# Optimization experiments

Hardware: AMD Instinct MI355X
Metric: run time of the kernel (lower is better)

## Reference

```python
import jax, jax.numpy as jnp
import numpy as np

KW = 3          # kernel_width
PAD = (KW - 1) // 2


def setup_inputs() -> dict:
    key = jax.random.key(0)
    ks = jax.random.split(key, 7)
    B, QL, KL, QS, KS = 16, 1024, 1024, 512, 512
    q = jax.random.normal(ks[0], (B, QL, QS), dtype=jnp.float32)
    k = jax.random.normal(ks[1], (B, KL, KS), dtype=jnp.float32)
    # torch Linear weights: [out_features, in_features]
    Wk = jax.random.normal(ks[2], (KS * KW, QS), dtype=jnp.float32) * (1.0 / np.sqrt(QS))
    bk = jax.random.normal(ks[3], (KS * KW,), dtype=jnp.float32) * 0.02
    Wb = jax.random.normal(ks[4], (1, QS), dtype=jnp.float32) * (1.0 / np.sqrt(QS))
    bb = jax.random.normal(ks[5], (1,), dtype=jnp.float32) * 0.02
    bias_b = jax.random.normal(ks[6], (1,), dtype=jnp.float32)
    return {"q": q, "k": k, "Wk": Wk, "bk": bk, "Wb": Wb, "bb": bb, "bias_b": bias_b}


def reference(q, k, Wk, bk, Wb, bb, bias_b):
    B, QL, QS = q.shape
    _, KL, KS = k.shape
    # per-query dynamic kernels: [B, QL, KS, KW]
    kernel = (jnp.einsum('biq,oq->bio', q, Wk) + bk).reshape(B, QL, KS, KW)
    # per-query scalar bias: [B, QL]
    bias = (jnp.einsum('biq,oq->bio', q, Wb) + bb)[..., 0]
    # banded multiply-accumulate, equivalent to grouped conv1d with groups=B
    k_pad = jnp.pad(k, ((0, 0), (PAD, PAD), (0, 0)))  # [B, KL+KW-1, KS]
    # windows[b, j, t, c] = k_pad[b, j+t, c]  -> [B, KL, KW, KS]
    windows = jnp.stack([k_pad[:, t:t + KL, :] for t in range(KW)], axis=2)
    scores = jnp.einsum('bict,bjtc->bij', kernel, windows)
    return scores + bias[:, :, None] + bias_b[0]
```

## Files before the change

kernel.cpp:

```cpp
#include <hip/hip_runtime.h>

typedef unsigned short ushort_t;
typedef unsigned int uint32;
typedef __bf16 bf16x8 __attribute__((ext_vector_type(8)));
typedef float f32x4 __attribute__((ext_vector_type(4)));
typedef float f4 __attribute__((ext_vector_type(4)));
typedef unsigned short us4 __attribute__((ext_vector_type(4)));


__device__ __forceinline__ ushort_t f2bf(float f) {
    uint32 u = __builtin_bit_cast(uint32, f);
    u = (u + 0x7fffu + ((u >> 16) & 1u)) >> 16;
    return (ushort_t)u;
}

#define SB0() __builtin_amdgcn_sched_barrier(0)
#define SBAR() __builtin_amdgcn_s_barrier()
#define VMCNT(n) asm volatile("s_waitcnt vmcnt(" #n ")" ::: "memory")
#define LGKM0_SB() do { asm volatile("s_waitcnt lgkmcnt(0)" ::: "memory"); SB0(); } while (0)

#define AS1 __attribute__((address_space(1)))
#define AS3 __attribute__((address_space(3)))

__global__ __launch_bounds__(256) void prep_all(const float* __restrict__ q,
                                                const float* __restrict__ Wb,
                                                const float* __restrict__ bb,
                                                const float* __restrict__ k,
                                                const float* __restrict__ Wk,
                                                const float* __restrict__ bk,
                                                ushort_t* __restrict__ qb,
                                                float* __restrict__ biasw,
                                                ushort_t* __restrict__ kbp,
                                                ushort_t* __restrict__ wkb,
                                                float* __restrict__ bkp) {
    const int tid = threadIdx.x;
    if (blockIdx.x < 4096) {
        const int lane = tid & 63, wid = tid >> 6;
        const int m = blockIdx.x * 4 + wid;
        const float* qrow = q + (size_t)m * 512;

        f4 v0 = *(const f4*)(qrow + lane * 4);
        f4 v1 = *(const f4*)(qrow + 256 + lane * 4);
        f4 w0 = *(const f4*)(Wb + lane * 4);
        f4 w1 = *(const f4*)(Wb + 256 + lane * 4);

        float dot = v0[0]*w0[0] + v0[1]*w0[1] + v0[2]*w0[2] + v0[3]*w0[3]
                  + v1[0]*w1[0] + v1[1]*w1[1] + v1[2]*w1[2] + v1[3]*w1[3];

        us4 o0, o1;
        o0[0]=f2bf(v0[0]); o0[1]=f2bf(v0[1]); o0[2]=f2bf(v0[2]); o0[3]=f2bf(v0[3]);
        o1[0]=f2bf(v1[0]); o1[1]=f2bf(v1[1]); o1[2]=f2bf(v1[2]); o1[3]=f2bf(v1[3]);
        *(us4*)(qb + (size_t)m * 512 + lane * 4) = o0;
        *(us4*)(qb + (size_t)m * 512 + 256 + lane * 4) = o1;

        #pragma unroll
        for (int off = 32; off >= 1; off >>= 1) dot += __shfl_xor(dot, off);
        if (lane == 0) biasw[m] = dot + bb[0];
        return;
    }
    const int gid = (blockIdx.x - 4096) * 256 + tid;
    if (gid < 1536) bkp[gid] = bk[(gid & 511) * 3 + (gid >> 9)];

    const int KG = (16 * 1024 * 512) / 4;
    const int PG = (16 * 2 * 512) / 4;

    if (gid < KG) {
        const int e = gid * 4;
        const int b = e >> 19;
        const int rem = e & ((1 << 19) - 1);
        const int row = rem >> 9, c = rem & 511;
        f4 v = *(const f4*)(k + e);
        us4 o; o[0]=f2bf(v[0]); o[1]=f2bf(v[1]); o[2]=f2bf(v[2]); o[3]=f2bf(v[3]);
        *(us4*)(kbp + ((size_t)b * 1026 + row + 1) * 512 + c) = o;
    } else if (gid < KG + PG) {
        const int p = gid - KG;
        const int b = p >> 8, off = p & 255;
        const int row = (off < 128) ? 0 : 1025;
        const int c = (off & 127) * 4;
        us4 z; z[0]=0; z[1]=0; z[2]=0; z[3]=0;
        *(us4*)(kbp + ((size_t)b * 1026 + row) * 512 + c) = z;
    } else {
        const int w = gid - KG - PG;
        const int n = w >> 7;
        const int c = (w & 127) * 4;
        const int o = (n & 511) * 3 + (n >> 9);
        f4 v = *(const f4*)(Wk + (size_t)o * 512 + c);
        us4 ov; ov[0]=f2bf(v[0]); ov[1]=f2bf(v[1]); ov[2]=f2bf(v[2]); ov[3]=f2bf(v[3]);
        *(us4*)(wkb + (size_t)n * 512 + c) = ov;
    }
}

template<int NINST>
__device__ __forceinline__ void stage_half(const char* base, int ld, char* dst, int tid) {
    #pragma unroll
    for (int inst = 0; inst < NINST; ++inst) {
        const int idx = inst * 512 + tid;
        const int row = idx >> 2;
        const int scol = ((idx & 3) ^ ((row >> 1) & 3)) << 4;
        __builtin_amdgcn_global_load_lds(
            (const AS1 void*)(base + (size_t)row * (size_t)ld + scol),
            (AS3 void*)(dst + (size_t)(inst * 512 + (tid & ~63)) * 16),
            16, 0, 0);
    }
}

#define CLUSTER16_G2(AF, BF, njb)                                            \
    __builtin_amdgcn_s_setprio(1);                                           \
    _Pragma("unroll")                                                        \
    for (int i_ = 0; i_ < 8; ++i_)                                           \
        _Pragma("unroll")                                                    \
        for (int j_ = 0; j_ < 2; ++j_)                                       \
            acc[i_][(njb) + j_] = __builtin_amdgcn_mfma_f32_16x16x32_bf16(   \
                AF[i_], BF[j_], acc[i_][(njb) + j_], 0, 0, 0);               \
    __builtin_amdgcn_s_setprio(0);                                           \
    SB0();

#define CLUSTER16_G1(AF, BF)                                                 \
    __builtin_amdgcn_s_setprio(1);                                           \
    _Pragma("unroll")                                                        \
    for (int i_ = 0; i_ < 4; ++i_)                                           \
        _Pragma("unroll")                                                    \
        for (int j_ = 0; j_ < 4; ++j_)                                       \
            acc[i_][j_] = __builtin_amdgcn_mfma_f32_16x16x32_bf16(           \
                AF[i_], BF[j_], acc[i_][j_], 0, 0, 0);                       \
    __builtin_amdgcn_s_setprio(0);                                           \
    SB0();

__global__ __launch_bounds__(512, 2) void gemm1(const ushort_t* __restrict__ qb,
                                                const ushort_t* __restrict__ wkb,
                                                const float* __restrict__ bkp,
                                                ushort_t* __restrict__ coef) {
    __shared__ alignas(16) char lds[147456];
    const int tid = threadIdx.x;
    const int l = tid & 63, wid = tid >> 6;
    const int wr = wid >> 2, wc = wid & 3;
    int bid = blockIdx.x;
    bid = (bid & 7) * 96 + (bid >> 3);
    const int mt = bid & 127, nt = bid >> 7;
    const int mbase = mt * 128, nbase = nt * 256;

    const char* Ag = (const char*)(qb + (size_t)mbase * 512);
    const char* Bg = (const char*)(wkb + (size_t)nbase * 512);

    const int r15 = l & 15, q = l >> 4;
    const int swz = ((q ^ (r15 >> 1)) & 3) << 4;
    const int laneA = (wr * 64 + r15) * 64 + swz;
    const int laneB = (wc * 64 + r15) * 64 + swz;

    f32x4 acc[4][4];
    #pragma unroll
    for (int mi = 0; mi < 4; ++mi)
        #pragma unroll
        for (int ni = 0; ni < 4; ++ni)
            #pragma unroll
            for (int r = 0; r < 4; ++r) acc[mi][ni][r] = 0.f;

    stage_half<1>(Ag, 1024, lds, tid);
    stage_half<2>(Bg, 1024, lds + 16384, tid);
    stage_half<1>(Ag + 64, 1024, lds + 8192, tid);
    stage_half<2>(Bg + 64, 1024, lds + 32768, tid);
    stage_half<1>(Ag + 128, 1024, lds + 49152, tid);
    stage_half<2>(Bg + 128, 1024, lds + 49152 + 16384, tid);
    stage_half<1>(Ag + 192, 1024, lds + 49152 + 8192, tid);
    stage_half<2>(Bg + 192, 1024, lds + 49152 + 32768, tid);
    VMCNT(9);
    SBAR(); SB0();

    for (int t = 0; t < 8; ++t) {
        const char* R = lds + (t % 3) * 49152;
        char* W       = lds + ((t + 2) % 3) * 49152;
        const int tn2 = (t + 2 < 8) ? t + 2 : 7;
        const size_t off2 = (size_t)tn2 * 128;

        bf16x8 A0[4], B0[4];
        #pragma unroll
        for (int i = 0; i < 4; ++i) A0[i] = *(const bf16x8*)(R + laneA + i * 1024);
        #pragma unroll
        for (int j = 0; j < 4; ++j) B0[j] = *(const bf16x8*)(R + 16384 + laneB + j * 1024);
        stage_half<1>(Ag + off2, 1024, W, tid);
        stage_half<2>(Bg + off2, 1024, W + 16384, tid);
        VMCNT(9);
        SBAR();
        LGKM0_SB();
        CLUSTER16_G1(A0, B0)

        #pragma unroll
        for (int i = 0; i < 4; ++i) A0[i] = *(const bf16x8*)(R + 8192 + laneA + i * 1024);
        #pragma unroll
        for (int j = 0; j < 4; ++j) B0[j] = *(const bf16x8*)(R + 32768 + laneB + j * 1024);
        stage_half<1>(Ag + off2 + 64, 1024, W + 8192, tid);
        stage_half<2>(Bg + off2 + 64, 1024, W + 32768, tid);
        VMCNT(9);
        SBAR();
        LGKM0_SB();
        CLUSTER16_G1(A0, B0)
    }

    #pragma unroll
    for (int ni = 0; ni < 4; ++ni) {
        const int ncol = nbase + wc * 64 + ni * 16 + r15;
        const float bkv = bkp[ncol];
        #pragma unroll
        for (int mi = 0; mi < 4; ++mi) {
            const int mrow0 = mbase + wr * 64 + mi * 16 + q * 4;
            #pragma unroll
            for (int r = 0; r < 4; ++r)
                coef[(size_t)(mrow0 + r) * 1536 + ncol] = f2bf(acc[mi][ni][r] + bkv);
        }
    }
}

__global__ __launch_bounds__(512, 2) void gemm2(const ushort_t* __restrict__ coef,
                                                const ushort_t* __restrict__ kbp,
                                                const float* __restrict__ biasw,
                                                const float* __restrict__ bias_b,
                                                float* __restrict__ out) {
    __shared__ alignas(16) char lds[131072];
    const int tid = threadIdx.x;
    const int l = tid & 63, wid = tid >> 6;
    const int wr = wid >> 2, wc = wid & 3;
    int bid = blockIdx.x;
    bid = (bid & 7) * 32 + (bid >> 3);
    const int jt = bid & 3, it = (bid >> 2) & 3, b = bid >> 4;
    const int ibase = it * 256, jbase = jt * 256;

    const char* Ag = (const char*)(coef + ((size_t)b * 1024 + ibase) * 1536);
    const char* Bg = (const char*)(kbp + ((size_t)b * 1026 + jbase) * 512);

    const int r15 = l & 15, q = l >> 4;
    const int swz = ((q ^ (r15 >> 1)) & 3) << 4;
    const int laneA = (wr * 128 + r15) * 64 + swz;
    const int laneB = (wc * 64 + r15) * 64 + swz;

    f32x4 acc[8][4];
    #pragma unroll
    for (int mi = 0; mi < 8; ++mi)
        #pragma unroll
        for (int ni = 0; ni < 4; ++ni)
            #pragma unroll
            for (int r = 0; r < 4; ++r) acc[mi][ni][r] = 0.f;

    stage_half<2>(Ag, 3072, lds, tid);
    stage_half<2>(Bg, 1024, lds + 32768, tid);
    stage_half<2>(Ag + 64, 3072, lds + 16384, tid);
    stage_half<2>(Bg + 64, 1024, lds + 49152, tid);
    VMCNT(4);
    SBAR(); SB0();

    for (int t = 0; t < 24; ++t) {
        const char* R = lds + ((t & 1) << 16);
        char* W       = lds + (((t + 1) & 1) << 16);
        const int tn = (t < 23) ? t + 1 : t;
        const size_t aoff = (size_t)tn * 128;
        const size_t boff = (size_t)(tn >> 3) * 1024 + (size_t)(tn & 7) * 128;

        bf16x8 A0[8], B0[2], B1[2];
        #pragma unroll
        for (int i = 0; i < 8; ++i) A0[i] = *(const bf16x8*)(R + laneA + i * 1024);
        B0[0] = *(const bf16x8*)(R + 32768 + laneB);
        B0[1] = *(const bf16x8*)(R + 32768 + laneB + 1024);
        stage_half<2>(Ag + aoff, 3072, W, tid);
        SBAR();
        LGKM0_SB();
        CLUSTER16_G2(A0, B0, 0)

        B1[0] = *(const bf16x8*)(R + 32768 + laneB + 2048);
        B1[1] = *(const bf16x8*)(R + 32768 + laneB + 3072);
        stage_half<2>(Bg + boff, 1024, W + 32768, tid);
        VMCNT(4);
        SBAR();
        LGKM0_SB();
        CLUSTER16_G2(A0, B1, 2)

        #pragma unroll
        for (int i = 0; i < 8; ++i) A0[i] = *(const bf16x8*)(R + 16384 + laneA + i * 1024);
        B0[0] = *(const bf16x8*)(R + 49152 + laneB);
        B0[1] = *(const bf16x8*)(R + 49152 + laneB + 1024);
        stage_half<2>(Ag + aoff + 64, 3072, W + 16384, tid);
        SBAR();
        LGKM0_SB();
        CLUSTER16_G2(A0, B0, 0)

        B1[0] = *(const bf16x8*)(R + 49152 + laneB + 2048);
        B1[1] = *(const bf16x8*)(R + 49152 + laneB + 3072);
        stage_half<2>(Bg + boff + 64, 1024, W + 49152, tid);
        VMCNT(4);
        SBAR();
        LGKM0_SB();
        CLUSTER16_G2(A0, B1, 2)
    }

    const float bb0v = bias_b[0];
    #pragma unroll
    for (int mi = 0; mi < 8; ++mi) {
        const int irow0 = ibase + wr * 128 + mi * 16 + q * 4;
        #pragma unroll
        for (int r = 0; r < 4; ++r) {
            const float bv = biasw[b * 1024 + irow0 + r] + bb0v;
            #pragma unroll
            for (int ni = 0; ni < 4; ++ni) {
                const int jcol = jbase + wc * 64 + ni * 16 + r15;
                out[((size_t)b << 20) + (size_t)(irow0 + r) * 1024 + jcol] = acc[mi][ni][r] + bv;
            }
        }
    }
}

extern "C" void kernel_launch(void* const* d_in, const int* in_sizes, int n_in,
                              void* d_out, int out_size, void* d_ws, size_t ws_size,
                              hipStream_t stream) {
    const float* q      = (const float*)d_in[0];
    const float* k      = (const float*)d_in[1];
    const float* Wk     = (const float*)d_in[2];
    const float* bk     = (const float*)d_in[3];
    const float* Wb     = (const float*)d_in[4];
    const float* bb     = (const float*)d_in[5];
    const float* bias_b = (const float*)d_in[6];
    float* out = (float*)d_out;

    ushort_t* ws   = (ushort_t*)d_ws;
    ushort_t* qb   = ws;
    ushort_t* kbp  = qb  + (size_t)16384 * 512;
    ushort_t* wkb  = kbp + (size_t)16 * 1026 * 512;
    ushort_t* coef = wkb + (size_t)1536 * 512;
    float*    biasw = (float*)(coef + (size_t)16384 * 1536);
    float*    bkp   = biasw + 16384;

    prep_all<<<13072, 256, 0, stream>>>(q, Wb, bb, k, Wk, bk, qb, biasw, kbp, wkb, bkp);
    gemm1<<<768, 512, 0, stream>>>(qb, wkb, bkp, coef);
    gemm2<<<256, 512, 0, stream>>>(coef, kbp, biasw, bias_b, out);
}
```

Before: 211.8 us.

## Shrink gemm1 to 128x128 tiles with 256 threads and simple double buffering

Replaces the 512-thread, 128x256-tile, triple-buffered gemm1 with a 256-thread, 128x128-tile kernel that double-buffers 64-wide K slices in 32KB of LDS and launches twice as many blocks. The aim is higher occupancy, three blocks per CU instead of two, and a simpler pipeline with less LDS pressure. In exchange it loses the tuned vmcnt-based prefetch distance and setprio scheduling, adds a full barrier every K step, and reloads the A tile twice as often across N tiles.

Result: slower. 218.4 us (+3.1%).

```diff
diff --git a/kernel.cpp b/kernel.cpp
--- a/kernel.cpp
+++ b/kernel.cpp
@@ -104,6 +104,20 @@
     }
 }
 
+template<int NINST>
+__device__ __forceinline__ void stage256(const char* base, int ld, char* dst, int tid) {
+    #pragma unroll
+    for (int inst = 0; inst < NINST; ++inst) {
+        const int idx = inst * 256 + tid;
+        const int row = idx >> 2;
+        const int scol = ((idx & 3) ^ ((row >> 1) & 3)) << 4;
+        __builtin_amdgcn_global_load_lds(
+            (const AS1 void*)(base + (size_t)row * (size_t)ld + scol),
+            (AS3 void*)(dst + (size_t)(inst * 256 + (tid & ~63)) * 16),
+            16, 0, 0);
+    }
+}
+
 #define CLUSTER16_G2(AF, BF, njb)                                            \
     __builtin_amdgcn_s_setprio(1);                                           \
     _Pragma("unroll")                                                        \
@@ -115,29 +129,18 @@
     __builtin_amdgcn_s_setprio(0);                                           \
     SB0();
 
-#define CLUSTER16_G1(AF, BF)                                                 \
-    __builtin_amdgcn_s_setprio(1);                                           \
-    _Pragma("unroll")                                                        \
-    for (int i_ = 0; i_ < 4; ++i_)                                           \
-        _Pragma("unroll")                                                    \
-        for (int j_ = 0; j_ < 4; ++j_)                                       \
-            acc[i_][j_] = __builtin_amdgcn_mfma_f32_16x16x32_bf16(           \
-                AF[i_], BF[j_], acc[i_][j_], 0, 0, 0);                       \
-    __builtin_amdgcn_s_setprio(0);                                           \
-    SB0();
-
-__global__ __launch_bounds__(512, 2) void gemm1(const ushort_t* __restrict__ qb,
+__global__ __launch_bounds__(256, 3) void gemm1(const ushort_t* __restrict__ qb,
                                                 const ushort_t* __restrict__ wkb,
                                                 const float* __restrict__ bkp,
                                                 ushort_t* __restrict__ coef) {
-    __shared__ alignas(16) char lds[147456];
+    __shared__ alignas(16) char lds[32768];
     const int tid = threadIdx.x;
     const int l = tid & 63, wid = tid >> 6;
-    const int wr = wid >> 2, wc = wid & 3;
+    const int wr = wid >> 1, wc = wid & 1;
     int bid = blockIdx.x;
-    bid = (bid & 7) * 96 + (bid >> 3);
+    bid = (bid & 7) * 192 + (bid >> 3);
     const int mt = bid & 127, nt = bid >> 7;
-    const int mbase = mt * 128, nbase = nt * 256;
+    const int mbase = mt * 128, nbase = nt * 128;
 
     const char* Ag = (const char*)(qb + (size_t)mbase * 512);
     const char* Bg = (const char*)(wkb + (size_t)nbase * 512);
@@ -155,45 +158,29 @@
             #pragma unroll
             for (int r = 0; r < 4; ++r) acc[mi][ni][r] = 0.f;
 
-    stage_half<1>(Ag, 1024, lds, tid);
-    stage_half<2>(Bg, 1024, lds + 16384, tid);
-    stage_half<1>(Ag + 64, 1024, lds + 8192, tid);
-    stage_half<2>(Bg + 64, 1024, lds + 32768, tid);
-    stage_half<1>(Ag + 128, 1024, lds + 49152, tid);
-    stage_half<2>(Bg + 128, 1024, lds + 49152 + 16384, tid);
-    stage_half<1>(Ag + 192, 1024, lds + 49152 + 8192, tid);
-    stage_half<2>(Bg + 192, 1024, lds + 49152 + 32768, tid);
-    VMCNT(9);
-    SBAR(); SB0();
-
-    for (int t = 0; t < 8; ++t) {
-        const char* R = lds + (t % 3) * 49152;
-        char* W       = lds + ((t + 2) % 3) * 49152;
-        const int tn2 = (t + 2 < 8) ? t + 2 : 7;
-        const size_t off2 = (size_t)tn2 * 128;
-
-        bf16x8 A0[4], B0[4];
-        #pragma unroll
-        for (int i = 0; i < 4; ++i) A0[i] = *(const bf16x8*)(R + laneA + i * 1024);
-        #pragma unroll
-        for (int j = 0; j < 4; ++j) B0[j] = *(const bf16x8*)(R + 16384 + laneB + j * 1024);
-        stage_half<1>(Ag + off2, 1024, W, tid);
-        stage_half<2>(Bg + off2, 1024, W + 16384, tid);
-        VMCNT(9);
-        SBAR();
-        LGKM0_SB();
-        CLUSTER16_G1(A0, B0)
-
-        #pragma unroll
-        for (int i = 0; i < 4; ++i) A0[i] = *(const bf16x8*)(R + 8192 + laneA + i * 1024);
-        #pragma unroll
-        for (int j = 0; j < 4; ++j) B0[j] = *(const bf16x8*)(R + 32768 + laneB + j * 1024);
-        stage_half<1>(Ag + off2 + 64, 1024, W + 8192, tid);
-        stage_half<2>(Bg + off2 + 64, 1024, W + 32768, tid);
-        VMCNT(9);
-        SBAR();
-        LGKM0_SB();
-        CLUSTER16_G1(A0, B0)
+    stage256<2>(Ag, 1024, lds, tid);
+    stage256<2>(Bg, 1024, lds + 8192, tid);
+    __syncthreads();
+
+    for (int t = 0; t < 16; ++t) {
+        const char* R = lds + ((t & 1) ? 16384 : 0);
+        char* W       = lds + ((t & 1) ? 0 : 16384);
+        const int tn = (t < 15) ? t + 1 : 15;
+
+        stage256<2>(Ag + (size_t)tn * 64, 1024, W, tid);
+        stage256<2>(Bg + (size_t)tn * 64, 1024, W + 8192, tid);
+
+        bf16x8 a[4], b[4];
+        #pragma unroll
+        for (int i = 0; i < 4; ++i) a[i] = *(const bf16x8*)(R + laneA + i * 1024);
+        #pragma unroll
+        for (int j = 0; j < 4; ++j) b[j] = *(const bf16x8*)(R + 8192 + laneB + j * 1024);
+        #pragma unroll
+        for (int i = 0; i < 4; ++i)
+            #pragma unroll
+            for (int j = 0; j < 4; ++j)
+                acc[i][j] = __builtin_amdgcn_mfma_f32_16x16x32_bf16(a[i], b[j], acc[i][j], 0, 0, 0);
+        __syncthreads();
     }
 
     #pragma unroll
@@ -327,6 +314,6 @@
     float*    bkp   = biasw + 16384;
 
     prep_all<<<13072, 256, 0, stream>>>(q, Wb, bb, k, Wk, bk, qb, biasw, kbp, wkb, bkp);
-    gemm1<<<768, 512, 0, stream>>>(qb, wkb, bkp, coef);
+    gemm1<<<1536, 256, 0, stream>>>(qb, wkb, bkp, coef);
     gemm2<<<256, 512, 0, stream>>>(coef, kbp, biasw, bias_b, out);
 }
```

## Restructure GEMM main loop with 4x4 MFMA clusters and fewer barriers

Applied to the files above, without the earlier changes.

Regroups each K-half of the score GEMM into two 4x4 MFMA clusters that split A rows into two halves and share the B fragments. This replaces the 8x2 clusters, which needed B reloaded between them. It cuts the per-iteration block barriers from four to two and drops the explicit lgkmcnt waits and scheduling barriers, so the compiler can interleave LDS reads, async global-to-LDS staging and MFMAs more freely. The intent is less barrier stall time and better overlap. The cost is more reliance on compiler-inserted waits and some change in register pressure.

Measured after the change: 214.3 us. No clear change (+1.2%).

```diff
diff --git a/kernel.cpp b/kernel.cpp
--- a/kernel.cpp
+++ b/kernel.cpp
@@ -104,17 +104,6 @@
     }
 }
 
-#define CLUSTER16_G2(AF, BF, njb)                                            \
-    __builtin_amdgcn_s_setprio(1);                                           \
-    _Pragma("unroll")                                                        \
-    for (int i_ = 0; i_ < 8; ++i_)                                           \
-        _Pragma("unroll")                                                    \
-        for (int j_ = 0; j_ < 2; ++j_)                                       \
-            acc[i_][(njb) + j_] = __builtin_amdgcn_mfma_f32_16x16x32_bf16(   \
-                AF[i_], BF[j_], acc[i_][(njb) + j_], 0, 0, 0);               \
-    __builtin_amdgcn_s_setprio(0);                                           \
-    SB0();
-
 #define CLUSTER16_G1(AF, BF)                                                 \
     __builtin_amdgcn_s_setprio(1);                                           \
     _Pragma("unroll")                                                        \
@@ -125,6 +114,16 @@
                 AF[i_], BF[j_], acc[i_][j_], 0, 0, 0);                       \
     __builtin_amdgcn_s_setprio(0);                                           \
     SB0();
+
+#define CLUSTER16_G2(AF, BF, r0)                                             \
+    __builtin_amdgcn_s_setprio(1);                                           \
+    _Pragma("unroll")                                                        \
+    for (int i_ = 0; i_ < 4; ++i_)                                           \
+        _Pragma("unroll")                                                    \
+        for (int j_ = 0; j_ < 4; ++j_)                                       \
+            acc[(r0) + i_][j_] = __builtin_amdgcn_mfma_f32_16x16x32_bf16(    \
+                AF[i_], BF[j_], acc[(r0) + i_][j_], 0, 0, 0);                \
+    __builtin_amdgcn_s_setprio(0);
 
 __global__ __launch_bounds__(512, 2) void gemm1(const ushort_t* __restrict__ qb,
                                                 const ushort_t* __restrict__ wkb,
@@ -245,7 +244,7 @@
     stage_half<2>(Ag + 64, 3072, lds + 16384, tid);
     stage_half<2>(Bg + 64, 1024, lds + 49152, tid);
     VMCNT(4);
-    SBAR(); SB0();
+    SBAR();
 
     for (int t = 0; t < 24; ++t) {
         const char* R = lds + ((t & 1) << 16);
@@ -254,40 +253,34 @@
         const size_t aoff = (size_t)tn * 128;
         const size_t boff = (size_t)(tn >> 3) * 1024 + (size_t)(tn & 7) * 128;
 
-        bf16x8 A0[8], B0[2], B1[2];
-        #pragma unroll
-        for (int i = 0; i < 8; ++i) A0[i] = *(const bf16x8*)(R + laneA + i * 1024);
-        B0[0] = *(const bf16x8*)(R + 32768 + laneB);
-        B0[1] = *(const bf16x8*)(R + 32768 + laneB + 1024);
+        bf16x8 A0[4], A1[4], B0[4], B1[4];
+        #pragma unroll
+        for (int i = 0; i < 4; ++i) A0[i] = *(const bf16x8*)(R + laneA + i * 1024);
+        #pragma unroll
+        for (int j = 0; j < 4; ++j) B0[j] = *(const bf16x8*)(R + 32768 + laneB + j * 1024);
         stage_half<2>(Ag + aoff, 3072, W, tid);
-        SBAR();
-        LGKM0_SB();
         CLUSTER16_G2(A0, B0, 0)
 
-        B1[0] = *(const bf16x8*)(R + 32768 + laneB + 2048);
-        B1[1] = *(const bf16x8*)(R + 32768 + laneB + 3072);
+        #pragma unroll
+        for (int i = 0; i < 4; ++i) A1[i] = *(const bf16x8*)(R + laneA + (4 + i) * 1024);
         stage_half<2>(Bg + boff, 1024, W + 32768, tid);
+        CLUSTER16_G2(A1, B0, 4)
         VMCNT(4);
         SBAR();
-        LGKM0_SB();
-        CLUSTER16_G2(A0, B1, 2)
-
-        #pragma unroll
-        for (int i = 0; i < 8; ++i) A0[i] = *(const bf16x8*)(R + 16384 + laneA + i * 1024);
-        B0[0] = *(const bf16x8*)(R + 49152 + laneB);
-        B0[1] = *(const bf16x8*)(R + 49152 + laneB + 1024);
+
+        #pragma unroll
+        for (int i = 0; i < 4; ++i) A0[i] = *(const bf16x8*)(R + 16384 + laneA + i * 1024);
+        #pragma unroll
+        for (int j = 0; j < 4; ++j) B1[j] = *(const bf16x8*)(R + 49152 + laneB + j * 1024);
         stage_half<2>(Ag + aoff + 64, 3072, W + 16384, tid);
-        SBAR();
-        LGKM0_SB();
-        CLUSTER16_G2(A0, B0, 0)
-
-        B1[0] = *(const bf16x8*)(R + 49152 + laneB + 2048);
-        B1[1] = *(const bf16x8*)(R + 49152 + laneB + 3072);
+        CLUSTER16_G2(A0, B1, 0)
+
+        #pragma unroll
+        for (int i = 0; i < 4; ++i) A1[i] = *(const bf16x8*)(R + 16384 + laneA + (4 + i) * 1024);
         stage_half<2>(Bg + boff + 64, 1024, W + 49152, tid);
+        CLUSTER16_G2(A1, B1, 4)
         VMCNT(4);
         SBAR();
-        LGKM0_SB();
-        CLUSTER16_G2(A0, B1, 2)
     }
 
     const float bb0v = bias_b[0];
```
